# Kernel tuning notes

Hardware: AMD Instinct MI355X
Metric: run time of the kernel (lower is better)

## Reference

```python
import jax, jax.numpy as jnp
import numpy as np

NUM_HEADS = 4
WINDOW_SIZE = 7
DILATION = 1


def local_mask(height, width, window_size, dilation):
    """[N, N] bool mask: True where token i may attend to token j (dilated 2D window)."""
    radius = window_size // 2
    rows = jnp.arange(height)
    cols = jnp.arange(width)
    r = jnp.repeat(rows, width)          # [N] row index of each flattened token
    c = jnp.tile(cols, height)           # [N] col index of each flattened token
    dr = r[:, None] - r[None, :]         # [N, N]
    dc = c[:, None] - c[None, :]
    within = (jnp.abs(dr) <= radius * dilation) & (jnpp_abs(dc) <= radius * dilation) if False else (
        (jnp.abs(dr) <= radius * dilation) & (jnp.abs(dc) <= radius * dilation)
    )
    on_grid = (dr % dilation == 0) & (dc % dilation == 0)
    return within & on_grid


def setup_inputs() -> dict:
    key = jax.random.key(0)
    kq, kk, kv = jax.random.split(key, 3)
    shape = (2, 64, 64, 64)  # (B, C, H, W)
    q = jax.random.normal(kq, shape, dtype=jnp.float32)
    k = jax.random.normal(kk, shape, dtype=jnp.float32)
    v = jax.random.normal(kv, shape, dtype=jnp.float32)
    return {"q": q, "k": k, "v": v}


def reference(q, k, v):
    B, C, H, W = q.shape
    nh = NUM_HEADS
    hd = C // nh
    N = H * W

    def to_seq(x):
        # (B, C, H, W) -> (B, nh, N, hd)
        x = x.reshape(B, nh, hd, H, W)
        return x.transpose(0, 1, 3, 4, 2).reshape(B, nh, N, hd)

    q_seq = to_seq(q)
    k_seq = to_seq(k)
    v_seq = to_seq(v)

    scale = 1.0 / jnp.sqrt(jnp.asarray(hd, dtype=q.dtype))
    scores = jnp.einsum("bhqd,bhkd->bhqk", q_seq, k_seq) * scale  # [B, nh, N, N]

    mask = local_mask(H, W, WINDOW_SIZE, DILATION)  # [N, N] bool
    neg = jnp.finfo(scores.dtype).min
    scores = jnp.where(mask[None, None, :, :], scores, neg)

    attn = jax.nn.softmax(scores, axis=-1)
    out = jnp.einsum("bhqk,bhkd->bhqd", attn, v_seq)  # [B, nh, N, hd]

    # (B, nh, N, hd) -> (B, C, H, W)
    out = out.reshape(B, nh, H, W, hd).transpose(0, 1, 4, 2, 3).reshape(B, C, H, W)
    return out
```

## Files before the change

### kernel.cpp

```cpp
#include <hip/hip_runtime.h>
#include <hip/hip_bf16.h>
#include <math.h>

#define HD  16
#define HW  4096
#define RAD 3

__global__ __launch_bounds__(512, 4)
void local_attn_kernel(const float* __restrict__ q,
                       const float* __restrict__ k,
                       const float* __restrict__ v,
                       float* __restrict__ out) {
    __shared__ float lds[14336];
    float* ldsK = lds;
    float* ldsV = lds + 7168;

    const int tid = threadIdx.x;
    const int c   = tid & 63;
    const int w   = tid >> 6;

    const int bid = blockIdx.x;
    const int r   = bid & 63;
    const int h   = (bid >> 6) & 3;
    const int b   = bid >> 8;
    const int base = (b * 4 + h) * (HD * HW);
    const int pos  = r * 64 + c;

    {
        const float* src = (w < 4) ? (k + base) : (v + base);
        float* dst = (w < 4) ? ldsK : ldsV;
        const int wl = w & 3;
#pragma unroll
        for (int ii = 0; ii < 7; ++ii) {
            int ci = wl + ii * 4;
            int s  = ci * 4 + (c >> 4);
            int d  = (int)((unsigned)s / 7u);
            int lr = s - d * 7;
            int rr = r - RAD + lr;
            rr = rr < 0 ? 0 : (rr > 63 ? 63 : rr);
            const float* g = src + d * HW + rr * 64 + (c & 15) * 4;
#if defined(__has_builtin) && __has_builtin(__builtin_amdgcn_global_load_lds)
            __builtin_amdgcn_global_load_lds(
                (const __attribute__((address_space(1))) void*)g,
                (__attribute__((address_space(3))) void*)&dst[ci * 256], 16, 0, 0);
#else
            *(float4*)&dst[ci * 256 + c * 4] = *(const float4*)g;
#endif
        }
    }

    float qv[HD];
    if (w < 7) {
#pragma unroll
        for (int d = 0; d < HD; ++d)
            qv[d] = q[base + d * HW + pos] * 0.25f;
    }

    int e2 = (c - RAD) & ~1;
    if (e2 < 0) e2 = 0;
    if (e2 > 56) e2 = 56;
    int lo = c - RAD; if (lo < 0) lo = 0;
    int hi = c + RAD; if (hi > 63) hi = 63;
    const int jlo = lo - e2, jhi = hi - e2;

    __syncthreads();

    float acc[HD];
#pragma unroll
    for (int d = 0; d < HD; ++d) acc[d] = 0.0f;
    float lsum = 0.0f;

    {
        const int dr = w;
        const int rr = r - RAD + dr;
        if (dr < 7 && (unsigned)rr < 64u) {
            float s8[8];
#pragma unroll
            for (int j = 0; j < 8; ++j) s8[j] = 0.0f;
#pragma unroll
            for (int d = 0; d < HD; ++d) {
                const float* kr = &ldsK[d * 448 + dr * 64 + e2];
                float2 k0 = *(const float2*)(kr);
                float2 k1 = *(const float2*)(kr + 2);
                float2 k2 = *(const float2*)(kr + 4);
                float2 k3 = *(const float2*)(kr + 6);
                s8[0] = fmaf(qv[d], k0.x, s8[0]);
                s8[1] = fmaf(qv[d], k0.y, s8[1]);
                s8[2] = fmaf(qv[d], k1.x, s8[2]);
                s8[3] = fmaf(qv[d], k1.y, s8[3]);
                s8[4] = fmaf(qv[d], k2.x, s8[4]);
                s8[5] = fmaf(qv[d], k2.y, s8[5]);
                s8[6] = fmaf(qv[d], k3.x, s8[6]);
                s8[7] = fmaf(qv[d], k3.y, s8[7]);
            }
#pragma unroll
            for (int j = 0; j < 8; ++j) {
                float p = __expf(s8[j]);
                p = (j >= jlo && j <= jhi) ? p : 0.0f;
                s8[j] = p;
                lsum += p;
            }
#pragma unroll
            for (int d = 0; d < HD; ++d) {
                const float* vr = &ldsV[d * 448 + dr * 64 + e2];
                float2 v0 = *(const float2*)(vr);
                float2 v1 = *(const float2*)(vr + 2);
                float2 v2 = *(const float2*)(vr + 4);
                float2 v3 = *(const float2*)(vr + 6);
                float a = acc[d];
                a = fmaf(s8[0], v0.x, a);
                a = fmaf(s8[1], v0.y, a);
                a = fmaf(s8[2], v1.x, a);
                a = fmaf(s8[3], v1.y, a);
                a = fmaf(s8[4], v2.x, a);
                a = fmaf(s8[5], v2.y, a);
                a = fmaf(s8[6], v3.x, a);
                a = fmaf(s8[7], v3.y, a);
                acc[d] = a;
            }
        }
    }

    __syncthreads();
#pragma unroll
    for (int d = 0; d < HD; ++d)
        lds[d * 512 + w * 64 + c] = acc[d];
    lds[8192 + w * 64 + c] = lsum;
    __syncthreads();

    float lt = 0.0f;
#pragma unroll
    for (int s = 0; s < 8; ++s)
        lt += lds[8192 + s * 64 + c];
    const float invl = 1.0f / lt;

#pragma unroll
    for (int i = 0; i < 2; ++i) {
        int d  = w * 2 + i;
        int a0 = d * 512 + c;
        float a = 0.0f;
#pragma unroll
        for (int s = 0; s < 8; ++s)
            a += lds[a0 + s * 64];
        out[base + d * HW + pos] = a * invl;
    }
}

extern "C" void kernel_launch(void* const* d_in, const int* in_sizes, int n_in,
                              void* d_out, int out_size, void* d_ws, size_t ws_size,
                              hipStream_t stream) {
    const float* q = (const float*)d_in[0];
    const float* k = (const float*)d_in[1];
    const float* v = (const float*)d_in[2];
    float* out = (float*)d_out;

    int queries = out_size / HD;
    int blocks  = queries / 64;
    local_attn_kernel<<<blocks, 512, 0, stream>>>(q, k, v, out);
}
```

Measured before the change: 12.43 us.

## Process two query rows per block to reuse staged K/V window rows

```diff
diff --git a/kernel.cpp b/kernel.cpp
--- a/kernel.cpp
+++ b/kernel.cpp
@@ -6,54 +6,52 @@
 #define HW  4096
 #define RAD 3
 
-__global__ __launch_bounds__(512, 4)
+__global__ __launch_bounds__(512, 2)
 void local_attn_kernel(const float* __restrict__ q,
                        const float* __restrict__ k,
                        const float* __restrict__ v,
                        float* __restrict__ out) {
-    __shared__ float lds[14336];
+    __shared__ float lds[17408];
     float* ldsK = lds;
-    float* ldsV = lds + 7168;
+    float* ldsV = lds + 8192;
 
     const int tid = threadIdx.x;
     const int c   = tid & 63;
     const int w   = tid >> 6;
 
     const int bid = blockIdx.x;
-    const int r   = bid & 63;
-    const int h   = (bid >> 6) & 3;
-    const int b   = bid >> 8;
+    const int r0  = (bid & 31) * 2;
+    const int h   = (bid >> 5) & 3;
+    const int b   = bid >> 7;
     const int base = (b * 4 + h) * (HD * HW);
-    const int pos  = r * 64 + c;
 
-    {
-        const float* src = (w < 4) ? (k + base) : (v + base);
-        float* dst = (w < 4) ? ldsK : ldsV;
-        const int wl = w & 3;
 #pragma unroll
-        for (int ii = 0; ii < 7; ++ii) {
-            int ci = wl + ii * 4;
-            int s  = ci * 4 + (c >> 4);
-            int d  = (int)((unsigned)s / 7u);
-            int lr = s - d * 7;
-            int rr = r - RAD + lr;
-            rr = rr < 0 ? 0 : (rr > 63 ? 63 : rr);
-            const float* g = src + d * HW + rr * 64 + (c & 15) * 4;
+    for (int ii = 0; ii < 8; ++ii) {
+        int ci = w * 8 + ii;
+        int cj = ci & 31;
+        const float* src = (ci < 32) ? (k + base) : (v + base);
+        float* dst = (ci < 32) ? ldsK : ldsV;
+        int s  = cj * 4 + (c >> 4);
+        int d  = s >> 3;
+        int hr = s & 7;
+        int rr = r0 - RAD + hr;
+        rr = rr < 0 ? 0 : (rr > 63 ? 63 : rr);
+        const float* g = src + d * HW + rr * 64 + (c & 15) * 4;
 #if defined(__has_builtin) && __has_builtin(__builtin_amdgcn_global_load_lds)
-            __builtin_amdgcn_global_load_lds(
-                (const __attribute__((address_space(1))) void*)g,
-                (__attribute__((address_space(3))) void*)&dst[ci * 256], 16, 0, 0);
+        __builtin_amdgcn_global_load_lds(
+            (const __attribute__((address_space(1))) void*)g,
+            (__attribute__((address_space(3))) void*)&dst[cj * 256], 16, 0, 0);
 #else
-            *(float4*)&dst[ci * 256 + c * 4] = *(const float4*)g;
+        *(float4*)&dst[cj * 256 + c * 4] = *(const float4*)g;
 #endif
-        }
     }
 
-    float qv[HD];
-    if (w < 7) {
+    const int pos0 = r0 * 64 + c;
+    float qv0[HD], qv1[HD];
 #pragma unroll
-        for (int d = 0; d < HD; ++d)
-            qv[d] = q[base + d * HW + pos] * 0.25f;
+    for (int d = 0; d < HD; ++d) {
+        qv0[d] = q[base + d * HW + pos0] * 0.25f;
+        qv1[d] = q[base + d * HW + pos0 + 64] * 0.25f;
     }
 
     int e2 = (c - RAD) & ~1;
@@ -65,84 +63,95 @@
 
     __syncthreads();
 
-    float acc[HD];
+    const int  rr     = r0 - RAD + w;
+    const bool rvalid = ((unsigned)rr < 64u);
+    const bool do0    = rvalid && (w <= 6);
+    const bool do1    = rvalid && (w >= 1);
+    const int  lrow   = w * 64 + e2;
+
+    float s0[8], s1[8];
 #pragma unroll
-    for (int d = 0; d < HD; ++d) acc[d] = 0.0f;
-    float lsum = 0.0f;
+    for (int j = 0; j < 8; ++j) { s0[j] = 0.0f; s1[j] = 0.0f; }
 
-    {
-        const int dr = w;
-        const int rr = r - RAD + dr;
-        if (dr < 7 && (unsigned)rr < 64u) {
-            float s8[8];
 #pragma unroll
-            for (int j = 0; j < 8; ++j) s8[j] = 0.0f;
+    for (int d = 0; d < HD; ++d) {
+        const float* kr = &ldsK[d * 512 + lrow];
+        float2 k0 = *(const float2*)(kr);
+        float2 k1 = *(const float2*)(kr + 2);
+        float2 k2 = *(const float2*)(kr + 4);
+        float2 k3 = *(const float2*)(kr + 6);
+        float q0 = qv0[d], q1 = qv1[d];
+        s0[0] = fmaf(q0, k0.x, s0[0]);  s1[0] = fmaf(q1, k0.x, s1[0]);
+        s0[1] = fmaf(q0, k0.y, s0[1]);  s1[1] = fmaf(q1, k0.y, s1[1]);
+        s0[2] = fmaf(q0, k1.x, s0[2]);  s1[2] = fmaf(q1, k1.x, s1[2]);
+        s0[3] = fmaf(q0, k1.y, s0[3]);  s1[3] = fmaf(q1, k1.y, s1[3]);
+        s0[4] = fmaf(q0, k2.x, s0[4]);  s1[4] = fmaf(q1, k2.x, s1[4]);
+        s0[5] = fmaf(q0, k2.y, s0[5]);  s1[5] = fmaf(q1, k2.y, s1[5]);
+        s0[6] = fmaf(q0, k3.x, s0[6]);  s1[6] = fmaf(q1, k3.x, s1[6]);
+        s0[7] = fmaf(q0, k3.y, s0[7]);  s1[7] = fmaf(q1, k3.y, s1[7]);
+    }
+
+    float l0 = 0.0f, l1 = 0.0f;
 #pragma unroll
-            for (int d = 0; d < HD; ++d) {
-                const float* kr = &ldsK[d * 448 + dr * 64 + e2];
-                float2 k0 = *(const float2*)(kr);
-                float2 k1 = *(const float2*)(kr + 2);
-                float2 k2 = *(const float2*)(kr + 4);
-                float2 k3 = *(const float2*)(kr + 6);
-                s8[0] = fmaf(qv[d], k0.x, s8[0]);
-                s8[1] = fmaf(qv[d], k0.y, s8[1]);
-                s8[2] = fmaf(qv[d], k1.x, s8[2]);
-                s8[3] = fmaf(qv[d], k1.y, s8[3]);
-                s8[4] = fmaf(qv[d], k2.x, s8[4]);
-                s8[5] = fmaf(qv[d], k2.y, s8[5]);
-                s8[6] = fmaf(qv[d], k3.x, s8[6]);
-                s8[7] = fmaf(qv[d], k3.y, s8[7]);
-            }
+    for (int j = 0; j < 8; ++j) {
+        bool okj = (j >= jlo) && (j <= jhi);
+        float e0 = __expf(s0[j]);
+        float e1 = __expf(s1[j]);
+        e0 = (okj && do0) ? e0 : 0.0f;
+        e1 = (okj && do1) ? e1 : 0.0f;
+        s0[j] = e0;  s1[j] = e1;
+        l0 += e0;    l1 += e1;
+    }
+
+    float acc0[HD], acc1[HD];
 #pragma unroll
-            for (int j = 0; j < 8; ++j) {
-                float p = __expf(s8[j]);
-                p = (j >= jlo && j <= jhi) ? p : 0.0f;
-                s8[j] = p;
-                lsum += p;
-            }
+    for (int d = 0; d < HD; ++d) { acc0[d] = 0.0f; acc1[d] = 0.0f; }
+
 #pragma unroll
-            for (int d = 0; d < HD; ++d) {
-                const float* vr = &ldsV[d * 448 + dr * 64 + e2];
-                float2 v0 = *(const float2*)(vr);
-                float2 v1 = *(const float2*)(vr + 2);
-                float2 v2 = *(const float2*)(vr + 4);
-                float2 v3 = *(const float2*)(vr + 6);
-                float a = acc[d];
-                a = fmaf(s8[0], v0.x, a);
-                a = fmaf(s8[1], v0.y, a);
-                a = fmaf(s8[2], v1.x, a);
-                a = fmaf(s8[3], v1.y, a);
-                a = fmaf(s8[4], v2.x, a);
-                a = fmaf(s8[5], v2.y, a);
-                a = fmaf(s8[6], v3.x, a);
-                a = fmaf(s8[7], v3.y, a);
-                acc[d] = a;
-            }
-        }
+    for (int d = 0; d < HD; ++d) {
+        const float* vr = &ldsV[d * 512 + lrow];
+        float2 v0 = *(const float2*)(vr);
+        float2 v1 = *(const float2*)(vr + 2);
+        float2 v2 = *(const float2*)(vr + 4);
+        float2 v3 = *(const float2*)(vr + 6);
+        float a0 = acc0[d], a1 = acc1[d];
+        a0 = fmaf(s0[0], v0.x, a0);  a1 = fmaf(s1[0], v0.x, a1);
+        a0 = fmaf(s0[1], v0.y, a0);  a1 = fmaf(s1[1], v0.y, a1);
+        a0 = fmaf(s0[2], v1.x, a0);  a1 = fmaf(s1[2], v1.x, a1);
+        a0 = fmaf(s0[3], v1.y, a0);  a1 = fmaf(s1[3], v1.y, a1);
+        a0 = fmaf(s0[4], v2.x, a0);  a1 = fmaf(s1[4], v2.x, a1);
+        a0 = fmaf(s0[5], v2.y, a0);  a1 = fmaf(s1[5], v2.y, a1);
+        a0 = fmaf(s0[6], v3.x, a0);  a1 = fmaf(s1[6], v3.x, a1);
+        a0 = fmaf(s0[7], v3.y, a0);  a1 = fmaf(s1[7], v3.y, a1);
+        acc0[d] = a0;  acc1[d] = a1;
     }
 
     __syncthreads();
 #pragma unroll
-    for (int d = 0; d < HD; ++d)
-        lds[d * 512 + w * 64 + c] = acc[d];
-    lds[8192 + w * 64 + c] = lsum;
+    for (int d = 0; d < HD; ++d) {
+        lds[d * 512 + w * 64 + c]         = acc0[d];
+        lds[(16 + d) * 512 + w * 64 + c]  = acc1[d];
+    }
+    lds[16384 + w * 64 + c]       = l0;
+    lds[16384 + 512 + w * 64 + c] = l1;
     __syncthreads();
 
+    const int qq = w >> 2;
+    const int dq = (w & 3) * 4;
     float lt = 0.0f;
 #pragma unroll
     for (int s = 0; s < 8; ++s)
-        lt += lds[8192 + s * 64 + c];
+        lt += lds[16384 + qq * 512 + s * 64 + c];
     const float invl = 1.0f / lt;
 
 #pragma unroll
-    for (int i = 0; i < 2; ++i) {
-        int d  = w * 2 + i;
-        int a0 = d * 512 + c;
+    for (int i = 0; i < 4; ++i) {
+        int d = dq + i;
         float a = 0.0f;
 #pragma unroll
         for (int s = 0; s < 8; ++s)
-            a += lds[a0 + s * 64];
-        out[base + d * HW + pos] = a * invl;
+            a += lds[(qq * 16 + d) * 512 + s * 64 + c];
+        out[base + d * HW + (r0 + qq) * 64 + c] = a * invl;
     }
 }
 
@@ -155,6 +164,6 @@
     float* out = (float*)d_out;
 
     int queries = out_size / HD;
-    int blocks  = queries / 64;
+    int blocks  = queries / 128;
     local_attn_kernel<<<blocks, 512, 0, stream>>>(q, k, v, out);
 }
```

New measurement: 10.67 us. 14.2% less time.
